# Performance work log

Measured on AMD Instinct MI355X. Metric: run time of the kernel, lower is better.

## Reference

```python
import jax, jax.numpy as jnp
import numpy as np


def _gcn_conv(x, edge_index, W, b):
    """PyG-style GCNConv: h = x @ W; out = D^-1/2 (A+I) D^-1/2 h + b."""
    N = x.shape[0]
    h = x @ W  # [N, F_out]
    # add self loops
    loops = jnp.arange(N, dtype=edge_index.dtype)
    src = jnp.concatenate([edge_index[0], loops])  # [E+N]
    dst = jnp.concatenate([edge_index[1], loops])  # [E+N]
    # symmetric normalization based on in-degree (incl. self loops)
    deg = jnp.zeros((N,), dtype=h.dtype).at[dst].add(1.0)
    dinv = jnp.where(deg > 0, jax.lax.rsqrt(deg), 0.0)
    norm = dinv[src] * dinv[dst]  # [E+N]
    # gather -> scale -> scatter-add
    msgs = h[src] * norm[:, None]  # [E+N, F_out]
    out = jax.ops.segment_sum(msgs, dst, num_segments=N)
    return out + b


def setup_inputs() -> dict:
    key = jax.random.key(0)
    k1, k2, k3, k4 = jax.random.split(key, 4)
    N, E, Cin, Ch, Cout = 50000, 800000, 128, 128, 64
    x = jax.random.normal(k1, (N, Cin), dtype=jnp.float32)
    edge_index = jax.random.randint(k2, (2, E), 0, N, dtype=jnp.int64)
    W1 = jax.random.normal(k3, (Cin, Ch), dtype=jnp.float32) / np.sqrt(Cin)
    b1 = jnp.zeros((Ch,), dtype=jnp.float32)
    W2 = jax.random.normal(k4, (Ch, Cout), dtype=jnp.float32) / np.sqrt(Ch)
    b2 = jnp.zeros((Cout,), dtype=jnp.float32)
    return {"x": x, "edge_index": edge_index, "W1": W1, "b1": b1, "W2": W2, "b2": b2}


def reference(x, edge_index, W1, b1, W2, b2):
    h = jax.nn.relu(_gcn_conv(x, edge_index, W1, b1))
    # F.dropout(training=self.training): eval mode -> identity
    return _gcn_conv(h, edge_index, W2, b2)
```

## Files before the change

### kernel.cpp

```cpp
#include <hip/hip_runtime.h>

typedef _Float16 f16;
typedef f16 f16x2 __attribute__((ext_vector_type(2)));
typedef f16 f16x8 __attribute__((ext_vector_type(8)));
typedef float f32x4 __attribute__((ext_vector_type(4)));

#define BSH 7
#define BN 128
#define CHUNK 4096
#define LCAP 4096
#define NBMAX 512
#define PMAX 512

__global__ __launch_bounds__(256) void k1(const float* __restrict__ x,
                                          const float* __restrict__ W1,
                                          const int* __restrict__ dst, f16* __restrict__ h,
                                          int* __restrict__ histG, int N, int E, int NB,
                                          int nblk) {
    __shared__ int hist[NBMAX];
    __shared__ f16 aT[64 * 136];
    __shared__ f16 bT[128 * 136];
    const int t = threadIdx.x;

    if ((int)blockIdx.x < nblk) {
        const int blk = blockIdx.x;
        for (int i = t; i < NB; i += 256) hist[i] = 0;
        __syncthreads();
        int lo = blk * CHUNK, hi = min(lo + CHUNK, E);
        for (int i = lo + t; i < hi; i += 256) atomicAdd(&hist[dst[i] >> BSH], 1);
        __syncthreads();
        for (int i = t; i < NB; i += 256) histG[(size_t)i * nblk + blk] = hist[i];
        return;
    }

    const int gb = blockIdx.x - nblk;
    const int row0 = gb * 64;
    {
        int r = t >> 2, s = (t & 3) * 32;
        bool ok = (row0 + r) < N;
        const float* xp = x + (size_t)(row0 + r) * 128 + s;
        f16* dp = &aT[r * 136 + s];
#pragma unroll
        for (int c = 0; c < 4; ++c) {
            f16x8 hv;
            if (ok) {
                float4 f0 = *(const float4*)(xp + c * 8);
                float4 f1 = *(const float4*)(xp + c * 8 + 4);
                hv[0] = (f16)f0.x; hv[1] = (f16)f0.y; hv[2] = (f16)f0.z; hv[3] = (f16)f0.w;
                hv[4] = (f16)f1.x; hv[5] = (f16)f1.y; hv[6] = (f16)f1.z; hv[7] = (f16)f1.w;
            } else {
#pragma unroll
                for (int j = 0; j < 8; ++j) hv[j] = (f16)0.f;
            }
            *(f16x8*)(dp + c * 8) = hv;
        }
    }
    for (int idx = t; idx < 128 * 128; idx += 256) {
        int k = idx >> 7, n = idx & 127;
        bT[n * 136 + k] = (f16)W1[idx];
    }
    __syncthreads();

    const int w = t >> 6, lane = t & 63, m15 = lane & 15, quad = lane >> 4;
    f32x4 acc[8];
#pragma unroll
    for (int c = 0; c < 8; ++c) acc[c] = (f32x4){0.f, 0.f, 0.f, 0.f};
    const f16* ar = &aT[(w * 16 + m15) * 136 + quad * 8];
#pragma unroll
    for (int k0 = 0; k0 < 128; k0 += 32) {
        f16x8 a = *(const f16x8*)(ar + k0);
#pragma unroll
        for (int c = 0; c < 8; ++c) {
            f16x8 b = *(const f16x8*)(&bT[(c * 16 + m15) * 136 + k0 + quad * 8]);
            acc[c] = __builtin_amdgcn_mfma_f32_16x16x32_f16(a, b, acc[c], 0, 0, 0);
        }
    }
#pragma unroll
    for (int c = 0; c < 8; ++c)
#pragma unroll
        for (int r = 0; r < 4; ++r) {
            int row = row0 + w * 16 + quad * 4 + r;
            if (row < N) h[(size_t)row * 128 + c * 16 + m15] = (f16)acc[c][r];
        }
}

__global__ __launch_bounds__(256) void scanA(int* __restrict__ a, int* __restrict__ bsum, int L) {
    __shared__ int tmp[256];
    int tid = threadIdx.x;
    int i = blockIdx.x * 256 + tid;
    int v = (i < L) ? a[i] : 0;
    tmp[tid] = v;
    __syncthreads();
    for (int o = 1; o < 256; o <<= 1) {
        int t2 = (tid >= o) ? tmp[tid - o] : 0;
        __syncthreads();
        tmp[tid] += t2;
        __syncthreads();
    }
    if (i < L) a[i] = tmp[tid] - v;
    if (tid == 255) bsum[blockIdx.x] = tmp[255];
}

__device__ __forceinline__ void scan_partials(const int* __restrict__ bsum, int nb2,
                                              int* excl , int* work ) {
    const int t = threadIdx.x & 255;
    for (int i = t; i < PMAX; i += 256) work[i] = (i < nb2) ? bsum[i] : 0;
    __syncthreads();
    for (int o = 1; o < PMAX; o <<= 1) {
        for (int i = t; i < PMAX; i += 256) excl[i] = work[i] + ((i >= o) ? work[i - o] : 0);
        __syncthreads();
        for (int i = t; i < PMAX; i += 256) work[i] = excl[i];
        __syncthreads();
    }
    for (int i = t; i < PMAX; i += 256) excl[i] = (i == 0) ? 0 : work[i - 1];
    __syncthreads();
}

__global__ __launch_bounds__(256) void place(const int* __restrict__ src,
                                             const int* __restrict__ dst,
                                             const int* __restrict__ histG,
                                             const int* __restrict__ bsum, int nb2,
                                             int* __restrict__ sorted, int E, int NB, int nblk) {
    __shared__ int excl[PMAX];
    __shared__ int work[PMAX];
    __shared__ int ofs[NBMAX];
    const int t = threadIdx.x, blk = blockIdx.x;
    scan_partials(bsum, nb2, excl, work);
    for (int i = t; i < NB; i += 256) {
        int idx = i * nblk + blk;
        ofs[i] = histG[idx] + excl[idx >> 8];
    }
    __syncthreads();
    int lo = blk * CHUNK, hi = min(lo + CHUNK, E);
    for (int i = lo + t; i < hi; i += 256) {
        int d = dst[i];
        int pos = atomicAdd(&ofs[d >> BSH], 1);
        sorted[pos] = (src[i] << BSH) | (d & (BN - 1));
    }
}

__global__ __launch_bounds__(256) void bucket_build(const int* __restrict__ histG,
                                                    const int* __restrict__ bsum, int nb2,
                                                    const int* __restrict__ sorted,
                                                    int* __restrict__ rowstart,
                                                    float* __restrict__ dinv,
                                                    int* __restrict__ csr_src, int N, int E,
                                                    int NB, int nblk) {
    __shared__ int ent[LCAP];
    __shared__ int hist[BN];
    __shared__ int lofs[BN];
    __shared__ int excl[PMAX];
    __shared__ int work[PMAX];
    const int b = blockIdx.x, t = threadIdx.x;
    scan_partials(bsum, nb2, excl, work);

    const int i0 = b * nblk;
    const int base = histG[i0] + excl[i0 >> 8];
    const int endb = (b == NB - 1) ? E : (histG[i0 + nblk] + excl[(i0 + nblk) >> 8]);
    int total = min(endb - base, LCAP);
    if (b == 0 && t == 0) rowstart[N] = E;

    for (int i = t; i < total; i += 256) ent[i] = sorted[base + i];
    if (t < BN) hist[t] = 0;
    __syncthreads();
    for (int i = t; i < total; i += 256) atomicAdd(&hist[ent[i] & (BN - 1)], 1);
    __syncthreads();
    if (t < BN) lofs[t] = hist[t];
    __syncthreads();
    for (int o = 1; o < BN; o <<= 1) {
        int v = (t < BN && t >= o) ? lofs[t - o] : 0;
        __syncthreads();
        if (t < BN) lofs[t] += v;
        __syncthreads();
    }
    if (t < BN) {
        int ex = lofs[t] - hist[t];
        int node = (b << BSH) + t;
        if (node < N) {
            rowstart[node] = base + ex;
            dinv[node] = rsqrtf((float)hist[t] + 1.0f);
        }
        lofs[t] = ex;
    }
    __syncthreads();
    for (int i = t; i < total; i += 256) {
        int e = ent[i];
        int pos = atomicAdd(&lofs[e & (BN - 1)], 1);
        csr_src[base + pos] = e >> BSH;
    }
}

__global__ __launch_bounds__(256) void gather1(const int* __restrict__ rowstart,
                                               const int* __restrict__ csr_src,
                                               const float* __restrict__ dinv,
                                               const f16* __restrict__ h,
                                               const float* __restrict__ b1,
                                               f16* __restrict__ r1, int N) {
    int node = (blockIdx.x * 256 + threadIdx.x) >> 6;
    int lane = threadIdx.x & 63;
    if (node >= N) return;
    int beg = rowstart[node], end = rowstart[node + 1];
    float dn = dinv[node];
    const f16x2* hv = (const f16x2*)h;

    f16x2 sv = hv[(size_t)node * 64 + lane];
    float ax = dn * (float)sv[0], ay = dn * (float)sv[1];
    int i = beg;
    for (; i + 4 <= end; i += 4) {
        int s0 = csr_src[i], s1 = csr_src[i + 1], s2 = csr_src[i + 2], s3 = csr_src[i + 3];
        float w0 = dinv[s0], w1 = dinv[s1], w2 = dinv[s2], w3 = dinv[s3];
        f16x2 v0 = hv[(size_t)s0 * 64 + lane];
        f16x2 v1 = hv[(size_t)s1 * 64 + lane];
        f16x2 v2 = hv[(size_t)s2 * 64 + lane];
        f16x2 v3 = hv[(size_t)s3 * 64 + lane];
        ax = fmaf(w0, (float)v0[0], ax); ay = fmaf(w0, (float)v0[1], ay);
        ax = fmaf(w1, (float)v1[0], ax); ay = fmaf(w1, (float)v1[1], ay);
        ax = fmaf(w2, (float)v2[0], ax); ay = fmaf(w2, (float)v2[1], ay);
        ax = fmaf(w3, (float)v3[0], ax); ay = fmaf(w3, (float)v3[1], ay);
    }
    for (; i < end; ++i) {
        int s = csr_src[i];
        float w = dinv[s];
        f16x2 v = hv[(size_t)s * 64 + lane];
        ax = fmaf(w, (float)v[0], ax);
        ay = fmaf(w, (float)v[1], ay);
    }
    float2 bb = ((const float2*)b1)[lane];
    float ox = fmaxf(fmaf(dn, ax, bb.x), 0.f);
    float oy = fmaxf(fmaf(dn, ay, bb.y), 0.f);
    ((f16x2*)r1)[(size_t)node * 64 + lane] = (f16x2){(f16)ox, (f16)oy};
}

__global__ __launch_bounds__(256) void gemm2(const f16* __restrict__ r1,
                                             const float* __restrict__ W2, f16* __restrict__ h2,
                                             int N) {
    __shared__ f16 aT[64 * 136];
    __shared__ f16 bT[64 * 136];
    const int t = threadIdx.x;
    const int row0 = blockIdx.x * 64;
    {
        int r = t >> 2, s = (t & 3) * 32;
        bool ok = (row0 + r) < N;
        const f16* rp = r1 + (size_t)(row0 + r) * 128 + s;
        f16* dp = &aT[r * 136 + s];
#pragma unroll
        for (int c = 0; c < 4; ++c) {
            f16x8 hv;
            if (ok) hv = *(const f16x8*)(rp + c * 8);
            else {
#pragma unroll
                for (int j = 0; j < 8; ++j) hv[j] = (f16)0.f;
            }
            *(f16x8*)(dp + c * 8) = hv;
        }
    }
    for (int idx = t; idx < 128 * 64; idx += 256) {
        int k = idx >> 6, n = idx & 63;
        bT[n * 136 + k] = (f16)W2[idx];
    }
    __syncthreads();

    const int w = t >> 6, lane = t & 63, m15 = lane & 15, quad = lane >> 4;
    f32x4 acc[4];
#pragma unroll
    for (int c = 0; c < 4; ++c) acc[c] = (f32x4){0.f, 0.f, 0.f, 0.f};
    const f16* ar = &aT[(w * 16 + m15) * 136 + quad * 8];
#pragma unroll
    for (int k0 = 0; k0 < 128; k0 += 32) {
        f16x8 a = *(const f16x8*)(ar + k0);
#pragma unroll
        for (int c = 0; c < 4; ++c) {
            f16x8 b = *(const f16x8*)(&bT[(c * 16 + m15) * 136 + k0 + quad * 8]);
            acc[c] = __builtin_amdgcn_mfma_f32_16x16x32_f16(a, b, acc[c], 0, 0, 0);
        }
    }
#pragma unroll
    for (int c = 0; c < 4; ++c)
#pragma unroll
        for (int r = 0; r < 4; ++r) {
            int row = row0 + w * 16 + quad * 4 + r;
            if (row < N) h2[(size_t)row * 64 + c * 16 + m15] = (f16)acc[c][r];
        }
}

__global__ __launch_bounds__(256) void gather2(const int* __restrict__ rowstart,
                                               const int* __restrict__ csr_src,
                                               const float* __restrict__ dinv,
                                               const f16* __restrict__ h2,
                                               const float* __restrict__ b2,
                                               float* __restrict__ out, int N) {
    int pair = (blockIdx.x * 256 + threadIdx.x) >> 6;
    int lane = threadIdx.x & 63;
    int sub = lane >> 5, l32 = lane & 31;
    int node = pair * 2 + sub;
    if (node >= N) return;
    int beg = rowstart[node], end = rowstart[node + 1];
    float dn = dinv[node];
    const f16x2* h2v = (const f16x2*)h2;

    f16x2 sv = h2v[(size_t)node * 32 + l32];
    float ax = dn * (float)sv[0], ay = dn * (float)sv[1];
    int i = beg;
    for (; i + 4 <= end; i += 4) {
        int s0 = csr_src[i], s1 = csr_src[i + 1], s2 = csr_src[i + 2], s3 = csr_src[i + 3];
        float w0 = dinv[s0], w1 = dinv[s1], w2 = dinv[s2], w3 = dinv[s3];
        f16x2 v0 = h2v[(size_t)s0 * 32 + l32];
        f16x2 v1 = h2v[(size_t)s1 * 32 + l32];
        f16x2 v2 = h2v[(size_t)s2 * 32 + l32];
        f16x2 v3 = h2v[(size_t)s3 * 32 + l32];
        ax = fmaf(w0, (float)v0[0], ax); ay = fmaf(w0, (float)v0[1], ay);
        ax = fmaf(w1, (float)v1[0], ax); ay = fmaf(w1, (float)v1[1], ay);
        ax = fmaf(w2, (float)v2[0], ax); ay = fmaf(w2, (float)v2[1], ay);
        ax = fmaf(w3, (float)v3[0], ax); ay = fmaf(w3, (float)v3[1], ay);
    }
    for (; i < end; ++i) {
        int s = csr_src[i];
        float w = dinv[s];
        f16x2 v = h2v[(size_t)s * 32 + l32];
        ax = fmaf(w, (float)v[0], ax);
        ay = fmaf(w, (float)v[1], ay);
    }
    float2 bb = ((const float2*)b2)[l32];
    float2 o;
    o.x = fmaf(dn, ax, bb.x);
    o.y = fmaf(dn, ay, bb.y);
    ((float2*)out)[(size_t)node * 32 + l32] = o;
}

extern "C" void kernel_launch(void* const* d_in, const int* in_sizes, int n_in,
                              void* d_out, int out_size, void* d_ws, size_t ws_size,
                              hipStream_t stream) {
    const float* x  = (const float*)d_in[0];
    const int*   ei = (const int*)d_in[1];
    const float* W1 = (const float*)d_in[2];
    const float* b1 = (const float*)d_in[3];
    const float* W2 = (const float*)d_in[4];
    const float* b2 = (const float*)d_in[5];

    const int N = in_sizes[0] / 128;
    const int E = in_sizes[1] / 2;
    const int* src = ei;
    const int* dst = ei + E;
    const int NB   = (N + BN - 1) >> BSH;
    const int nblk = (E + CHUNK - 1) / CHUNK;
    const int L    = NB * nblk;
    const int nb2  = (L + 255) / 256;

    char* p = (char*)d_ws;
    auto bump = [&](size_t bytes) {
        char* r = p;
        p += (bytes + 255) & ~(size_t)255;
        return r;
    };
    int*   histG    = (int*)bump((size_t)L * 4);
    int*   bsum     = (int*)bump((size_t)nb2 * 4);
    int*   sorted   = (int*)bump((size_t)E * 4);
    int*   rowstart = (int*)bump((size_t)(N + 1) * 4);
    float* dinv     = (float*)bump((size_t)N * 4);
    int*   csr_src  = (int*)bump((size_t)E * 4);
    f16*   h        = (f16*)bump((size_t)N * 128 * 2);
    f16*   r1       = (f16*)bump((size_t)N * 128 * 2);
    f16*   h2       = (f16*)bump((size_t)N * 64 * 2);
    float* out      = (float*)d_out;

    k1<<<nblk + (N + 63) / 64, 256, 0, stream>>>(x, W1, dst, h, histG, N, E, NB, nblk);
    scanA<<<nb2, 256, 0, stream>>>(histG, bsum, L);
    place<<<nblk, 256, 0, stream>>>(src, dst, histG, bsum, nb2, sorted, E, NB, nblk);
    bucket_build<<<NB, 256, 0, stream>>>(histG, bsum, nb2, sorted, rowstart, dinv, csr_src, N, E,
                                         NB, nblk);
    gather1<<<(N + 3) / 4, 256, 0, stream>>>(rowstart, csr_src, dinv, h, b1, r1, N);
    gemm2<<<(N + 63) / 64, 256, 0, stream>>>(r1, W2, h2, N);
    gather2<<<(N / 2 + 3) / 4, 256, 0, stream>>>(rowstart, csr_src, dinv, h2, b2, out, N);
}
```

Baseline: 194.0 us.

## Build CSR with global atomics and prescale features by source dinv

Measured after the change: 233.4 us. 1.2x slower.

```diff
diff --git a/kernel.cpp b/kernel.cpp
--- a/kernel.cpp
+++ b/kernel.cpp
@@ -5,34 +5,102 @@
 typedef f16 f16x8 __attribute__((ext_vector_type(8)));
 typedef float f32x4 __attribute__((ext_vector_type(4)));
 
-#define BSH 7
-#define BN 128
 #define CHUNK 4096
-#define LCAP 4096
-#define NBMAX 512
 #define PMAX 512
+
+__global__ __launch_bounds__(256) void degk(const int* __restrict__ dst, int* __restrict__ deg,
+                                            int E) {
+    int i = (blockIdx.x * 256 + threadIdx.x) * 4;
+    if (i + 4 <= E) {
+        int4 d = *(const int4*)(dst + i);
+        atomicAdd(&deg[d.x], 1);
+        atomicAdd(&deg[d.y], 1);
+        atomicAdd(&deg[d.z], 1);
+        atomicAdd(&deg[d.w], 1);
+    } else if (i < E) {
+        for (; i < E; ++i) atomicAdd(&deg[dst[i]], 1);
+    }
+}
+
+__global__ __launch_bounds__(256) void scanA(const int* __restrict__ in, int* __restrict__ outx,
+                                             int* __restrict__ bsum, int L) {
+    __shared__ int tmp[256];
+    int tid = threadIdx.x;
+    int i = blockIdx.x * 256 + tid;
+    int v = (i < L) ? in[i] : 0;
+    tmp[tid] = v;
+    __syncthreads();
+    for (int o = 1; o < 256; o <<= 1) {
+        int t2 = (tid >= o) ? tmp[tid - o] : 0;
+        __syncthreads();
+        tmp[tid] += t2;
+        __syncthreads();
+    }
+    if (i < L) outx[i] = tmp[tid] - v;
+    if (tid == 255) bsum[blockIdx.x] = tmp[255];
+}
+
+__device__ __forceinline__ void scan_partials(const int* __restrict__ bsum, int nb2,
+                                              int* excl , int* work ) {
+    const int t = threadIdx.x & 255;
+    for (int i = t; i < PMAX; i += 256) work[i] = (i < nb2) ? bsum[i] : 0;
+    __syncthreads();
+    for (int o = 1; o < PMAX; o <<= 1) {
+        for (int i = t; i < PMAX; i += 256) excl[i] = work[i] + ((i >= o) ? work[i - o] : 0);
+        __syncthreads();
+        for (int i = t; i < PMAX; i += 256) work[i] = excl[i];
+        __syncthreads();
+    }
+    for (int i = t; i < PMAX; i += 256) excl[i] = (i == 0) ? 0 : work[i - 1];
+    __syncthreads();
+}
+
+__global__ __launch_bounds__(256) void finalize(const int* __restrict__ rowscan,
+                                                const int* __restrict__ bsum, int nb2,
+                                                const int* __restrict__ deg,
+                                                int* __restrict__ rowstart, int* __restrict__ ofs,
+                                                float* __restrict__ dinv, int N, int E) {
+    __shared__ int excl[PMAX];
+    __shared__ int work[PMAX];
+    scan_partials(bsum, nb2, excl, work);
+    int i = blockIdx.x * 256 + threadIdx.x;
+    if (i < N) {
+        int rs = rowscan[i] + excl[blockIdx.x];
+        rowstart[i] = rs;
+        ofs[i] = rs;
+        dinv[i] = rsqrtf((float)deg[i] + 1.0f);
+    }
+    if (i == 0) rowstart[N] = E;
+}
 
 __global__ __launch_bounds__(256) void k1(const float* __restrict__ x,
                                           const float* __restrict__ W1,
-                                          const int* __restrict__ dst, f16* __restrict__ h,
-                                          int* __restrict__ histG, int N, int E, int NB,
-                                          int nblk) {
-    __shared__ int hist[NBMAX];
+                                          const int* __restrict__ src, const int* __restrict__ dst,
+                                          int* __restrict__ ofs, int* __restrict__ csr_src,
+                                          const float* __restrict__ dinv, f16* __restrict__ h,
+                                          int N, int E, int nblk) {
+    const int t = threadIdx.x;
+
+    if ((int)blockIdx.x < nblk) {
+        const int base = blockIdx.x * CHUNK;
+        const int n = min(CHUNK, E - base);
+        for (int j = t * 4; j + 4 <= n; j += 1024) {
+            int4 d4 = *(const int4*)(dst + base + j);
+            int4 s4 = *(const int4*)(src + base + j);
+            csr_src[atomicAdd(&ofs[d4.x], 1)] = s4.x;
+            csr_src[atomicAdd(&ofs[d4.y], 1)] = s4.y;
+            csr_src[atomicAdd(&ofs[d4.z], 1)] = s4.z;
+            csr_src[atomicAdd(&ofs[d4.w], 1)] = s4.w;
+        }
+        if (t == 0) {
+            for (int j = n & ~3; j < n; ++j)
+                csr_src[atomicAdd(&ofs[dst[base + j]], 1)] = src[base + j];
+        }
+        return;
+    }
+
     __shared__ f16 aT[64 * 136];
     __shared__ f16 bT[128 * 136];
-    const int t = threadIdx.x;
-
-    if ((int)blockIdx.x < nblk) {
-        const int blk = blockIdx.x;
-        for (int i = t; i < NB; i += 256) hist[i] = 0;
-        __syncthreads();
-        int lo = blk * CHUNK, hi = min(lo + CHUNK, E);
-        for (int i = lo + t; i < hi; i += 256) atomicAdd(&hist[dst[i] >> BSH], 1);
-        __syncthreads();
-        for (int i = t; i < NB; i += 256) histG[(size_t)i * nblk + blk] = hist[i];
-        return;
-    }
-
     const int gb = blockIdx.x - nblk;
     const int row0 = gb * 64;
     {
@@ -75,119 +143,20 @@
             acc[c] = __builtin_amdgcn_mfma_f32_16x16x32_f16(a, b, acc[c], 0, 0, 0);
         }
     }
+    const int rbase = row0 + w * 16 + quad * 4;
+    float dv[4];
+#pragma unroll
+    for (int r = 0; r < 4; ++r) {
+        int row = rbase + r;
+        dv[r] = (row < N) ? dinv[row] : 0.f;
+    }
 #pragma unroll
     for (int c = 0; c < 8; ++c)
 #pragma unroll
         for (int r = 0; r < 4; ++r) {
-            int row = row0 + w * 16 + quad * 4 + r;
-            if (row < N) h[(size_t)row * 128 + c * 16 + m15] = (f16)acc[c][r];
-        }
-}
-
-__global__ __launch_bounds__(256) void scanA(int* __restrict__ a, int* __restrict__ bsum, int L) {
-    __shared__ int tmp[256];
-    int tid = threadIdx.x;
-    int i = blockIdx.x * 256 + tid;
-    int v = (i < L) ? a[i] : 0;
-    tmp[tid] = v;
-    __syncthreads();
-    for (int o = 1; o < 256; o <<= 1) {
-        int t2 = (tid >= o) ? tmp[tid - o] : 0;
-        __syncthreads();
-        tmp[tid] += t2;
-        __syncthreads();
-    }
-    if (i < L) a[i] = tmp[tid] - v;
-    if (tid == 255) bsum[blockIdx.x] = tmp[255];
-}
-
-__device__ __forceinline__ void scan_partials(const int* __restrict__ bsum, int nb2,
-                                              int* excl , int* work ) {
-    const int t = threadIdx.x & 255;
-    for (int i = t; i < PMAX; i += 256) work[i] = (i < nb2) ? bsum[i] : 0;
-    __syncthreads();
-    for (int o = 1; o < PMAX; o <<= 1) {
-        for (int i = t; i < PMAX; i += 256) excl[i] = work[i] + ((i >= o) ? work[i - o] : 0);
-        __syncthreads();
-        for (int i = t; i < PMAX; i += 256) work[i] = excl[i];
-        __syncthreads();
-    }
-    for (int i = t; i < PMAX; i += 256) excl[i] = (i == 0) ? 0 : work[i - 1];
-    __syncthreads();
-}
-
-__global__ __launch_bounds__(256) void place(const int* __restrict__ src,
-                                             const int* __restrict__ dst,
-                                             const int* __restrict__ histG,
-                                             const int* __restrict__ bsum, int nb2,
-                                             int* __restrict__ sorted, int E, int NB, int nblk) {
-    __shared__ int excl[PMAX];
-    __shared__ int work[PMAX];
-    __shared__ int ofs[NBMAX];
-    const int t = threadIdx.x, blk = blockIdx.x;
-    scan_partials(bsum, nb2, excl, work);
-    for (int i = t; i < NB; i += 256) {
-        int idx = i * nblk + blk;
-        ofs[i] = histG[idx] + excl[idx >> 8];
-    }
-    __syncthreads();
-    int lo = blk * CHUNK, hi = min(lo + CHUNK, E);
-    for (int i = lo + t; i < hi; i += 256) {
-        int d = dst[i];
-        int pos = atomicAdd(&ofs[d >> BSH], 1);
-        sorted[pos] = (src[i] << BSH) | (d & (BN - 1));
-    }
-}
-
-__global__ __launch_bounds__(256) void bucket_build(const int* __restrict__ histG,
-                                                    const int* __restrict__ bsum, int nb2,
-                                                    const int* __restrict__ sorted,
-                                                    int* __restrict__ rowstart,
-                                                    float* __restrict__ dinv,
-                                                    int* __restrict__ csr_src, int N, int E,
-                                                    int NB, int nblk) {
-    __shared__ int ent[LCAP];
-    __shared__ int hist[BN];
-    __shared__ int lofs[BN];
-    __shared__ int excl[PMAX];
-    __shared__ int work[PMAX];
-    const int b = blockIdx.x, t = threadIdx.x;
-    scan_partials(bsum, nb2, excl, work);
-
-    const int i0 = b * nblk;
-    const int base = histG[i0] + excl[i0 >> 8];
-    const int endb = (b == NB - 1) ? E : (histG[i0 + nblk] + excl[(i0 + nblk) >> 8]);
-    int total = min(endb - base, LCAP);
-    if (b == 0 && t == 0) rowstart[N] = E;
-
-    for (int i = t; i < total; i += 256) ent[i] = sorted[base + i];
-    if (t < BN) hist[t] = 0;
-    __syncthreads();
-    for (int i = t; i < total; i += 256) atomicAdd(&hist[ent[i] & (BN - 1)], 1);
-    __syncthreads();
-    if (t < BN) lofs[t] = hist[t];
-    __syncthreads();
-    for (int o = 1; o < BN; o <<= 1) {
-        int v = (t < BN && t >= o) ? lofs[t - o] : 0;
-        __syncthreads();
-        if (t < BN) lofs[t] += v;
-        __syncthreads();
-    }
-    if (t < BN) {
-        int ex = lofs[t] - hist[t];
-        int node = (b << BSH) + t;
-        if (node < N) {
-            rowstart[node] = base + ex;
-            dinv[node] = rsqrtf((float)hist[t] + 1.0f);
-        }
-        lofs[t] = ex;
-    }
-    __syncthreads();
-    for (int i = t; i < total; i += 256) {
-        int e = ent[i];
-        int pos = atomicAdd(&lofs[e & (BN - 1)], 1);
-        csr_src[base + pos] = e >> BSH;
-    }
+            int row = rbase + r;
+            if (row < N) h[(size_t)row * 128 + c * 16 + m15] = (f16)(acc[c][r] * dv[r]);
+        }
 }
 
 __global__ __launch_bounds__(256) void gather1(const int* __restrict__ rowstart,
@@ -196,7 +165,7 @@
                                                const f16* __restrict__ h,
                                                const float* __restrict__ b1,
                                                f16* __restrict__ r1, int N) {
-    int node = (blockIdx.x * 256 + threadIdx.x) >> 6;
+    int node = __builtin_amdgcn_readfirstlane((int)((blockIdx.x * 256 + threadIdx.x) >> 6));
     int lane = threadIdx.x & 63;
     if (node >= N) return;
     int beg = rowstart[node], end = rowstart[node + 1];
@@ -204,30 +173,28 @@
     const f16x2* hv = (const f16x2*)h;
 
     f16x2 sv = hv[(size_t)node * 64 + lane];
-    float ax = dn * (float)sv[0], ay = dn * (float)sv[1];
+    float ax = (float)sv[0], ay = (float)sv[1];
     int i = beg;
     for (; i + 4 <= end; i += 4) {
         int s0 = csr_src[i], s1 = csr_src[i + 1], s2 = csr_src[i + 2], s3 = csr_src[i + 3];
-        float w0 = dinv[s0], w1 = dinv[s1], w2 = dinv[s2], w3 = dinv[s3];
         f16x2 v0 = hv[(size_t)s0 * 64 + lane];
         f16x2 v1 = hv[(size_t)s1 * 64 + lane];
         f16x2 v2 = hv[(size_t)s2 * 64 + lane];
         f16x2 v3 = hv[(size_t)s3 * 64 + lane];
-        ax = fmaf(w0, (float)v0[0], ax); ay = fmaf(w0, (float)v0[1], ay);
-        ax = fmaf(w1, (float)v1[0], ax); ay = fmaf(w1, (float)v1[1], ay);
-        ax = fmaf(w2, (float)v2[0], ax); ay = fmaf(w2, (float)v2[1], ay);
-        ax = fmaf(w3, (float)v3[0], ax); ay = fmaf(w3, (float)v3[1], ay);
+        ax += (float)v0[0]; ay += (float)v0[1];
+        ax += (float)v1[0]; ay += (float)v1[1];
+        ax += (float)v2[0]; ay += (float)v2[1];
+        ax += (float)v3[0]; ay += (float)v3[1];
     }
     for (; i < end; ++i) {
         int s = csr_src[i];
-        float w = dinv[s];
         f16x2 v = hv[(size_t)s * 64 + lane];
-        ax = fmaf(w, (float)v[0], ax);
-        ay = fmaf(w, (float)v[1], ay);
+        ax += (float)v[0];
+        ay += (float)v[1];
     }
     float2 bb = ((const float2*)b1)[lane];
-    float ox = fmaxf(fmaf(dn, ax, bb.x), 0.f);
-    float oy = fmaxf(fmaf(dn, ay, bb.y), 0.f);
+    float ox = dn * fmaxf(fmaf(dn, ax, bb.x), 0.f);
+    float oy = dn * fmaxf(fmaf(dn, ay, bb.y), 0.f);
     ((f16x2*)r1)[(size_t)node * 64 + lane] = (f16x2){(f16)ox, (f16)oy};
 }
 
@@ -299,26 +266,24 @@
     const f16x2* h2v = (const f16x2*)h2;
 
     f16x2 sv = h2v[(size_t)node * 32 + l32];
-    float ax = dn * (float)sv[0], ay = dn * (float)sv[1];
+    float ax = (float)sv[0], ay = (float)sv[1];
     int i = beg;
     for (; i + 4 <= end; i += 4) {
         int s0 = csr_src[i], s1 = csr_src[i + 1], s2 = csr_src[i + 2], s3 = csr_src[i + 3];
-        float w0 = dinv[s0], w1 = dinv[s1], w2 = dinv[s2], w3 = dinv[s3];
         f16x2 v0 = h2v[(size_t)s0 * 32 + l32];
         f16x2 v1 = h2v[(size_t)s1 * 32 + l32];
         f16x2 v2 = h2v[(size_t)s2 * 32 + l32];
         f16x2 v3 = h2v[(size_t)s3 * 32 + l32];
-        ax = fmaf(w0, (float)v0[0], ax); ay = fmaf(w0, (float)v0[1], ay);
-        ax = fmaf(w1, (float)v1[0], ax); ay = fmaf(w1, (float)v1[1], ay);
-        ax = fmaf(w2, (float)v2[0], ax); ay = fmaf(w2, (float)v2[1], ay);
-        ax = fmaf(w3, (float)v3[0], ax); ay = fmaf(w3, (float)v3[1], ay);
+        ax += (float)v0[0]; ay += (float)v0[1];
+        ax += (float)v1[0]; ay += (float)v1[1];
+        ax += (float)v2[0]; ay += (float)v2[1];
+        ax += (float)v3[0]; ay += (float)v3[1];
     }
     for (; i < end; ++i) {
         int s = csr_src[i];
-        float w = dinv[s];
         f16x2 v = h2v[(size_t)s * 32 + l32];
-        ax = fmaf(w, (float)v[0], ax);
-        ay = fmaf(w, (float)v[1], ay);
+        ax += (float)v[0];
+        ay += (float)v[1];
     }
     float2 bb = ((const float2*)b2)[l32];
     float2 o;
@@ -341,10 +306,8 @@
     const int E = in_sizes[1] / 2;
     const int* src = ei;
     const int* dst = ei + E;
-    const int NB   = (N + BN - 1) >> BSH;
     const int nblk = (E + CHUNK - 1) / CHUNK;
-    const int L    = NB * nblk;
-    const int nb2  = (L + 255) / 256;
+    const int nb2  = (N + 255) / 256;
 
     char* p = (char*)d_ws;
     auto bump = [&](size_t bytes) {
@@ -352,10 +315,11 @@
         p += (bytes + 255) & ~(size_t)255;
         return r;
     };
-    int*   histG    = (int*)bump((size_t)L * 4);
+    int*   deg      = (int*)bump((size_t)N * 4);
+    int*   rowscan  = (int*)bump((size_t)N * 4);
     int*   bsum     = (int*)bump((size_t)nb2 * 4);
-    int*   sorted   = (int*)bump((size_t)E * 4);
     int*   rowstart = (int*)bump((size_t)(N + 1) * 4);
+    int*   ofs      = (int*)bump((size_t)N * 4);
     float* dinv     = (float*)bump((size_t)N * 4);
     int*   csr_src  = (int*)bump((size_t)E * 4);
     f16*   h        = (f16*)bump((size_t)N * 128 * 2);
@@ -363,11 +327,12 @@
     f16*   h2       = (f16*)bump((size_t)N * 64 * 2);
     float* out      = (float*)d_out;
 
-    k1<<<nblk + (N + 63) / 64, 256, 0, stream>>>(x, W1, dst, h, histG, N, E, NB, nblk);
-    scanA<<<nb2, 256, 0, stream>>>(histG, bsum, L);
-    place<<<nblk, 256, 0, stream>>>(src, dst, histG, bsum, nb2, sorted, E, NB, nblk);
-    bucket_build<<<NB, 256, 0, stream>>>(histG, bsum, nb2, sorted, rowstart, dinv, csr_src, N, E,
-                                         NB, nblk);
+    hipMemsetAsync(deg, 0, (size_t)N * 4, stream);
+    degk<<<(E / 4 + 255) / 256, 256, 0, stream>>>(dst, deg, E);
+    scanA<<<nb2, 256, 0, stream>>>(deg, rowscan, bsum, N);
+    finalize<<<nb2, 256, 0, stream>>>(rowscan, bsum, nb2, deg, rowstart, ofs, dinv, N, E);
+    k1<<<nblk + (N + 63) / 64, 256, 0, stream>>>(x, W1, src, dst, ofs, csr_src, dinv, h, N, E,
+                                                 nblk);
     gather1<<<(N + 3) / 4, 256, 0, stream>>>(rowstart, csr_src, dinv, h, b1, r1, N);
     gemm2<<<(N + 63) / 64, 256, 0, stream>>>(r1, W2, h2, N);
     gather2<<<(N / 2 + 3) / 4, 256, 0, stream>>>(rowstart, csr_src, dinv, h2, b2, out, N);
```

## Restructure pipeline: fuse place with GEMM1, pre-transpose weights, fold dinv into gather1

Applied to the files above, without the earlier changes.

Result: faster. 181.3 us, median of 2 (-6.6%).

```diff
diff --git a/kernel.cpp b/kernel.cpp
--- a/kernel.cpp
+++ b/kernel.cpp
@@ -2,6 +2,7 @@
 
 typedef _Float16 f16;
 typedef f16 f16x2 __attribute__((ext_vector_type(2)));
+typedef f16 f16x4 __attribute__((ext_vector_type(4)));
 typedef f16 f16x8 __attribute__((ext_vector_type(8)));
 typedef float f32x4 __attribute__((ext_vector_type(4)));
 
@@ -12,24 +13,100 @@
 #define NBMAX 512
 #define PMAX 512
 
+__global__ __launch_bounds__(256) void degh(const int* __restrict__ dst, int* __restrict__ histG,
+                                            const float* __restrict__ W1,
+                                            const float* __restrict__ W2, f16* __restrict__ w1t,
+                                            f16* __restrict__ w2t, int E, int NB, int nblk) {
+    const int t = threadIdx.x, blk = blockIdx.x;
+    if (blk < nblk) {
+        __shared__ int hist[NBMAX];
+        for (int i = t; i < NB; i += 256) hist[i] = 0;
+        __syncthreads();
+        int lo = blk * CHUNK, hi = min(lo + CHUNK, E);
+        for (int i = lo + t; i < hi; i += 256) atomicAdd(&hist[dst[i] >> BSH], 1);
+        __syncthreads();
+        for (int i = t; i < NB; i += 256) histG[(size_t)i * nblk + blk] = hist[i];
+        return;
+    }
+    if (blk == nblk) {
+        for (int idx = t; idx < 128 * 128; idx += 256) {
+            int n = idx >> 7, k = idx & 127;
+            w1t[idx] = (f16)W1[k * 128 + n];
+        }
+        return;
+    }
+    for (int idx = t; idx < 64 * 128; idx += 256) {
+        int n = idx >> 7, k = idx & 127;
+        w2t[idx] = (f16)W2[k * 64 + n];
+    }
+}
+
+__global__ __launch_bounds__(256) void scanA(int* __restrict__ a, int* __restrict__ bsum, int L) {
+    __shared__ int tmp[256];
+    int tid = threadIdx.x;
+    int i = blockIdx.x * 256 + tid;
+    int v = (i < L) ? a[i] : 0;
+    tmp[tid] = v;
+    __syncthreads();
+    for (int o = 1; o < 256; o <<= 1) {
+        int t2 = (tid >= o) ? tmp[tid - o] : 0;
+        __syncthreads();
+        tmp[tid] += t2;
+        __syncthreads();
+    }
+    if (i < L) a[i] = tmp[tid] - v;
+    if (tid == 255) bsum[blockIdx.x] = tmp[255];
+}
+
+__device__ __forceinline__ void scan_partials(const int* __restrict__ bsum, int nb2,
+                                              int* excl , int* work ) {
+    const int t = threadIdx.x & 255;
+    for (int i = t; i < PMAX; i += 256) work[i] = (i < nb2) ? bsum[i] : 0;
+    __syncthreads();
+    for (int o = 1; o < PMAX; o <<= 1) {
+        for (int i = t; i < PMAX; i += 256) excl[i] = work[i] + ((i >= o) ? work[i - o] : 0);
+        __syncthreads();
+        for (int i = t; i < PMAX; i += 256) work[i] = excl[i];
+        __syncthreads();
+    }
+    for (int i = t; i < PMAX; i += 256) excl[i] = (i == 0) ? 0 : work[i - 1];
+    __syncthreads();
+}
+
 __global__ __launch_bounds__(256) void k1(const float* __restrict__ x,
-                                          const float* __restrict__ W1,
-                                          const int* __restrict__ dst, f16* __restrict__ h,
-                                          int* __restrict__ histG, int N, int E, int NB,
-                                          int nblk) {
-    __shared__ int hist[NBMAX];
-    __shared__ f16 aT[64 * 136];
-    __shared__ f16 bT[128 * 136];
+                                          const f16* __restrict__ w1t,
+                                          const int* __restrict__ src, const int* __restrict__ dst,
+                                          const int* __restrict__ histG,
+                                          const int* __restrict__ bsum, int nb2,
+                                          int* __restrict__ sorted, f16* __restrict__ h, int N,
+                                          int E, int NB, int nblk) {
+    __shared__ union SM {
+        struct {
+            f16 aT[64 * 136];
+            f16 bT[128 * 136];
+        } g;
+        struct {
+            int excl[PMAX];
+            int work[PMAX];
+            int ofs[NBMAX];
+        } p;
+    } sm;
     const int t = threadIdx.x;
 
     if ((int)blockIdx.x < nblk) {
         const int blk = blockIdx.x;
-        for (int i = t; i < NB; i += 256) hist[i] = 0;
+        scan_partials(bsum, nb2, sm.p.excl, sm.p.work);
+        for (int i = t; i < NB; i += 256) {
+            int idx = i * nblk + blk;
+            sm.p.ofs[i] = histG[idx] + sm.p.excl[idx >> 8];
+        }
         __syncthreads();
         int lo = blk * CHUNK, hi = min(lo + CHUNK, E);
-        for (int i = lo + t; i < hi; i += 256) atomicAdd(&hist[dst[i] >> BSH], 1);
-        __syncthreads();
-        for (int i = t; i < NB; i += 256) histG[(size_t)i * nblk + blk] = hist[i];
+        for (int i = lo + t; i < hi; i += 256) {
+            int d = dst[i];
+            int pos = atomicAdd(&sm.p.ofs[d >> BSH], 1);
+            sorted[pos] = (src[i] << BSH) | (d & (BN - 1));
+        }
         return;
     }
 
@@ -39,7 +116,7 @@
         int r = t >> 2, s = (t & 3) * 32;
         bool ok = (row0 + r) < N;
         const float* xp = x + (size_t)(row0 + r) * 128 + s;
-        f16* dp = &aT[r * 136 + s];
+        f16* dp = &sm.g.aT[r * 136 + s];
 #pragma unroll
         for (int c = 0; c < 4; ++c) {
             f16x8 hv;
@@ -55,9 +132,9 @@
             *(f16x8*)(dp + c * 8) = hv;
         }
     }
-    for (int idx = t; idx < 128 * 128; idx += 256) {
-        int k = idx >> 7, n = idx & 127;
-        bT[n * 136 + k] = (f16)W1[idx];
+    for (int idx = t; idx < 128 * 16; idx += 256) {
+        int n = idx >> 4, c = idx & 15;
+        *(f16x8*)&sm.g.bT[n * 136 + c * 8] = *(const f16x8*)&w1t[n * 128 + c * 8];
     }
     __syncthreads();
 
@@ -65,13 +142,13 @@
     f32x4 acc[8];
 #pragma unroll
     for (int c = 0; c < 8; ++c) acc[c] = (f32x4){0.f, 0.f, 0.f, 0.f};
-    const f16* ar = &aT[(w * 16 + m15) * 136 + quad * 8];
+    const f16* ar = &sm.g.aT[(w * 16 + m15) * 136 + quad * 8];
 #pragma unroll
     for (int k0 = 0; k0 < 128; k0 += 32) {
         f16x8 a = *(const f16x8*)(ar + k0);
 #pragma unroll
         for (int c = 0; c < 8; ++c) {
-            f16x8 b = *(const f16x8*)(&bT[(c * 16 + m15) * 136 + k0 + quad * 8]);
+            f16x8 b = *(const f16x8*)(&sm.g.bT[(c * 16 + m15) * 136 + k0 + quad * 8]);
             acc[c] = __builtin_amdgcn_mfma_f32_16x16x32_f16(a, b, acc[c], 0, 0, 0);
         }
     }
@@ -82,61 +159,6 @@
             int row = row0 + w * 16 + quad * 4 + r;
             if (row < N) h[(size_t)row * 128 + c * 16 + m15] = (f16)acc[c][r];
         }
-}
-
-__global__ __launch_bounds__(256) void scanA(int* __restrict__ a, int* __restrict__ bsum, int L) {
-    __shared__ int tmp[256];
-    int tid = threadIdx.x;
-    int i = blockIdx.x * 256 + tid;
-    int v = (i < L) ? a[i] : 0;
-    tmp[tid] = v;
-    __syncthreads();
-    for (int o = 1; o < 256; o <<= 1) {
-        int t2 = (tid >= o) ? tmp[tid - o] : 0;
-        __syncthreads();
-        tmp[tid] += t2;
-        __syncthreads();
-    }
-    if (i < L) a[i] = tmp[tid] - v;
-    if (tid == 255) bsum[blockIdx.x] = tmp[255];
-}
-
-__device__ __forceinline__ void scan_partials(const int* __restrict__ bsum, int nb2,
-                                              int* excl , int* work ) {
-    const int t = threadIdx.x & 255;
-    for (int i = t; i < PMAX; i += 256) work[i] = (i < nb2) ? bsum[i] : 0;
-    __syncthreads();
-    for (int o = 1; o < PMAX; o <<= 1) {
-        for (int i = t; i < PMAX; i += 256) excl[i] = work[i] + ((i >= o) ? work[i - o] : 0);
-        __syncthreads();
-        for (int i = t; i < PMAX; i += 256) work[i] = excl[i];
-        __syncthreads();
-    }
-    for (int i = t; i < PMAX; i += 256) excl[i] = (i == 0) ? 0 : work[i - 1];
-    __syncthreads();
-}
-
-__global__ __launch_bounds__(256) void place(const int* __restrict__ src,
-                                             const int* __restrict__ dst,
-                                             const int* __restrict__ histG,
-                                             const int* __restrict__ bsum, int nb2,
-                                             int* __restrict__ sorted, int E, int NB, int nblk) {
-    __shared__ int excl[PMAX];
-    __shared__ int work[PMAX];
-    __shared__ int ofs[NBMAX];
-    const int t = threadIdx.x, blk = blockIdx.x;
-    scan_partials(bsum, nb2, excl, work);
-    for (int i = t; i < NB; i += 256) {
-        int idx = i * nblk + blk;
-        ofs[i] = histG[idx] + excl[idx >> 8];
-    }
-    __syncthreads();
-    int lo = blk * CHUNK, hi = min(lo + CHUNK, E);
-    for (int i = lo + t; i < hi; i += 256) {
-        int d = dst[i];
-        int pos = atomicAdd(&ofs[d >> BSH], 1);
-        sorted[pos] = (src[i] << BSH) | (d & (BN - 1));
-    }
 }
 
 __global__ __launch_bounds__(256) void bucket_build(const int* __restrict__ histG,
@@ -196,43 +218,52 @@
                                                const f16* __restrict__ h,
                                                const float* __restrict__ b1,
                                                f16* __restrict__ r1, int N) {
-    int node = (blockIdx.x * 256 + threadIdx.x) >> 6;
+    int wid = (blockIdx.x * 256 + threadIdx.x) >> 6;
     int lane = threadIdx.x & 63;
+    int sub = lane >> 5, l32 = lane & 31;
+    int node = wid * 2 + sub;
     if (node >= N) return;
     int beg = rowstart[node], end = rowstart[node + 1];
     float dn = dinv[node];
-    const f16x2* hv = (const f16x2*)h;
-
-    f16x2 sv = hv[(size_t)node * 64 + lane];
-    float ax = dn * (float)sv[0], ay = dn * (float)sv[1];
+    const f16x4* hv = (const f16x4*)h;
+
+    f16x4 sv = hv[(size_t)node * 32 + l32];
+    float a0 = dn * (float)sv[0], a1 = dn * (float)sv[1];
+    float a2 = dn * (float)sv[2], a3 = dn * (float)sv[3];
     int i = beg;
     for (; i + 4 <= end; i += 4) {
         int s0 = csr_src[i], s1 = csr_src[i + 1], s2 = csr_src[i + 2], s3 = csr_src[i + 3];
         float w0 = dinv[s0], w1 = dinv[s1], w2 = dinv[s2], w3 = dinv[s3];
-        f16x2 v0 = hv[(size_t)s0 * 64 + lane];
-        f16x2 v1 = hv[(size_t)s1 * 64 + lane];
-        f16x2 v2 = hv[(size_t)s2 * 64 + lane];
-        f16x2 v3 = hv[(size_t)s3 * 64 + lane];
-        ax = fmaf(w0, (float)v0[0], ax); ay = fmaf(w0, (float)v0[1], ay);
-        ax = fmaf(w1, (float)v1[0], ax); ay = fmaf(w1, (float)v1[1], ay);
-        ax = fmaf(w2, (float)v2[0], ax); ay = fmaf(w2, (float)v2[1], ay);
-        ax = fmaf(w3, (float)v3[0], ax); ay = fmaf(w3, (float)v3[1], ay);
+        f16x4 v0 = hv[(size_t)s0 * 32 + l32];
+        f16x4 v1 = hv[(size_t)s1 * 32 + l32];
+        f16x4 v2 = hv[(size_t)s2 * 32 + l32];
+        f16x4 v3 = hv[(size_t)s3 * 32 + l32];
+        a0 = fmaf(w0, (float)v0[0], a0); a1 = fmaf(w0, (float)v0[1], a1);
+        a2 = fmaf(w0, (float)v0[2], a2); a3 = fmaf(w0, (float)v0[3], a3);
+        a0 = fmaf(w1, (float)v1[0], a0); a1 = fmaf(w1, (float)v1[1], a1);
+        a2 = fmaf(w1, (float)v1[2], a2); a3 = fmaf(w1, (float)v1[3], a3);
+        a0 = fmaf(w2, (float)v2[0], a0); a1 = fmaf(w2, (float)v2[1], a1);
+        a2 = fmaf(w2, (float)v2[2], a2); a3 = fmaf(w2, (float)v2[3], a3);
+        a0 = fmaf(w3, (float)v3[0], a0); a1 = fmaf(w3, (float)v3[1], a1);
+        a2 = fmaf(w3, (float)v3[2], a2); a3 = fmaf(w3, (float)v3[3], a3);
     }
     for (; i < end; ++i) {
         int s = csr_src[i];
         float w = dinv[s];
-        f16x2 v = hv[(size_t)s * 64 + lane];
-        ax = fmaf(w, (float)v[0], ax);
-        ay = fmaf(w, (float)v[1], ay);
-    }
-    float2 bb = ((const float2*)b1)[lane];
-    float ox = fmaxf(fmaf(dn, ax, bb.x), 0.f);
-    float oy = fmaxf(fmaf(dn, ay, bb.y), 0.f);
-    ((f16x2*)r1)[(size_t)node * 64 + lane] = (f16x2){(f16)ox, (f16)oy};
+        f16x4 v = hv[(size_t)s * 32 + l32];
+        a0 = fmaf(w, (float)v[0], a0); a1 = fmaf(w, (float)v[1], a1);
+        a2 = fmaf(w, (float)v[2], a2); a3 = fmaf(w, (float)v[3], a3);
+    }
+    float4 bb = ((const float4*)b1)[l32];
+    float o0 = dn * fmaxf(fmaf(dn, a0, bb.x), 0.f);
+    float o1 = dn * fmaxf(fmaf(dn, a1, bb.y), 0.f);
+    float o2 = dn * fmaxf(fmaf(dn, a2, bb.z), 0.f);
+    float o3 = dn * fmaxf(fmaf(dn, a3, bb.w), 0.f);
+    ((f16x4*)r1)[(size_t)node * 32 + l32] = (f16x4){(f16)o0, (f16)o1, (f16)o2, (f16)o3};
 }
 
 __global__ __launch_bounds__(256) void gemm2(const f16* __restrict__ r1,
-                                             const float* __restrict__ W2, f16* __restrict__ h2,
+                                             const f16* __restrict__ w2t, f16* __restrict__ h2,
                                              int N) {
     __shared__ f16 aT[64 * 136];
     __shared__ f16 bT[64 * 136];
@@ -254,9 +285,9 @@
             *(f16x8*)(dp + c * 8) = hv;
         }
     }
-    for (int idx = t; idx < 128 * 64; idx += 256) {
-        int k = idx >> 6, n = idx & 63;
-        bT[n * 136 + k] = (f16)W2[idx];
+    for (int idx = t; idx < 64 * 16; idx += 256) {
+        int n = idx >> 4, c = idx & 15;
+        *(f16x8*)&bT[n * 136 + c * 8] = *(const f16x8*)&w2t[n * 128 + c * 8];
     }
     __syncthreads();
 
@@ -289,42 +320,41 @@
                                                const f16* __restrict__ h2,
                                                const float* __restrict__ b2,
                                                float* __restrict__ out, int N) {
-    int pair = (blockIdx.x * 256 + threadIdx.x) >> 6;
+    int wid = (blockIdx.x * 256 + threadIdx.x) >> 6;
     int lane = threadIdx.x & 63;
-    int sub = lane >> 5, l32 = lane & 31;
-    int node = pair * 2 + sub;
+    int q = lane >> 4, l16 = lane & 15;
+    int node = wid * 4 + q;
     if (node >= N) return;
     int beg = rowstart[node], end = rowstart[node + 1];
     float dn = dinv[node];
-    const f16x2* h2v = (const f16x2*)h2;
-
-    f16x2 sv = h2v[(size_t)node * 32 + l32];
-    float ax = dn * (float)sv[0], ay = dn * (float)sv[1];
+    const f16x4* h2v = (const f16x4*)h2;
+
+    f16x4 sv = h2v[(size_t)node * 16 + l16];
+    float a0 = (float)sv[0], a1 = (float)sv[1], a2 = (float)sv[2], a3 = (float)sv[3];
     int i = beg;
     for (; i + 4 <= end; i += 4) {
         int s0 = csr_src[i], s1 = csr_src[i + 1], s2 = csr_src[i + 2], s3 = csr_src[i + 3];
-        float w0 = dinv[s0], w1 = dinv[s1], w2 = dinv[s2], w3 = dinv[s3];
-        f16x2 v0 = h2v[(size_t)s0 * 32 + l32];
-        f16x2 v1 = h2v[(size_t)s1 * 32 + l32];
-        f16x2 v2 = h2v[(size_t)s2 * 32 + l32];
-        f16x2 v3 = h2v[(size_t)s3 * 32 + l32];
-        ax = fmaf(w0, (float)v0[0], ax); ay = fmaf(w0, (float)v0[1], ay);
-        ax = fmaf(w1, (float)v1[0], ax); ay = fmaf(w1, (float)v1[1], ay);
-        ax = fmaf(w2, (float)v2[0], ax); ay = fmaf(w2, (float)v2[1], ay);
-        ax = fmaf(w3, (float)v3[0], ax); ay = fmaf(w3, (float)v3[1], ay);
+        f16x4 v0 = h2v[(size_t)s0 * 16 + l16];
+        f16x4 v1 = h2v[(size_t)s1 * 16 + l16];
+        f16x4 v2 = h2v[(size_t)s2 * 16 + l16];
+        f16x4 v3 = h2v[(size_t)s3 * 16 + l16];
+        a0 += (float)v0[0]; a1 += (float)v0[1]; a2 += (float)v0[2]; a3 += (float)v0[3];
+        a0 += (float)v1[0]; a1 += (float)v1[1]; a2 += (float)v1[2]; a3 += (float)v1[3];
+        a0 += (float)v2[0]; a1 += (float)v2[1]; a2 += (float)v2[2]; a3 += (float)v2[3];
+        a0 += (float)v3[0]; a1 += (float)v3[1]; a2 += (float)v3[2]; a3 += (float)v3[3];
     }
     for (; i < end; ++i) {
         int s = csr_src[i];
-        float w = dinv[s];
-        f16x2 v = h2v[(size_t)s * 32 + l32];
-        ax = fmaf(w, (float)v[0], ax);
-        ay = fmaf(w, (float)v[1], ay);
-    }
-    float2 bb = ((const float2*)b2)[l32];
-    float2 o;
-    o.x = fmaf(dn, ax, bb.x);
-    o.y = fmaf(dn, ay, bb.y);
-    ((float2*)out)[(size_t)node * 32 + l32] = o;
+        f16x4 v = h2v[(size_t)s * 16 + l16];
+        a0 += (float)v[0]; a1 += (float)v[1]; a2 += (float)v[2]; a3 += (float)v[3];
+    }
+    float4 bb = ((const float4*)b2)[l16];
+    float4 o;
+    o.x = fmaf(dn, a0, bb.x);
+    o.y = fmaf(dn, a1, bb.y);
+    o.z = fmaf(dn, a2, bb.z);
+    o.w = fmaf(dn, a3, bb.w);
+    ((float4*)out)[(size_t)node * 16 + l16] = o;
 }
 
 extern "C" void kernel_launch(void* const* d_in, const int* in_sizes, int n_in,
@@ -361,14 +391,17 @@
     f16*   h        = (f16*)bump((size_t)N * 128 * 2);
     f16*   r1       = (f16*)bump((size_t)N * 128 * 2);
     f16*   h2       = (f16*)bump((size_t)N * 64 * 2);
+    f16*   w1t      = (f16*)bump((size_t)128 * 128 * 2);
+    f16*   w2t      = (f16*)bump((size_t)64 * 128 * 2);
     float* out      = (float*)d_out;
 
-    k1<<<nblk + (N + 63) / 64, 256, 0, stream>>>(x, W1, dst, h, histG, N, E, NB, nblk);
+    degh<<<nblk + 2, 256, 0, stream>>>(dst, histG, W1, W2, w1t, w2t, E, NB, nblk);
     scanA<<<nb2, 256, 0, stream>>>(histG, bsum, L);
-    place<<<nblk, 256, 0, stream>>>(src, dst, histG, bsum, nb2, sorted, E, NB, nblk);
+    k1<<<nblk + (N + 63) / 64, 256, 0, stream>>>(x, w1t, src, dst, histG, bsum, nb2, sorted, h, N,
+                                                 E, NB, nblk);
     bucket_build<<<NB, 256, 0, stream>>>(histG, bsum, nb2, sorted, rowstart, dinv, csr_src, N, E,
                                          NB, nblk);
-    gather1<<<(N + 3) / 4, 256, 0, stream>>>(rowstart, csr_src, dinv, h, b1, r1, N);
-    gemm2<<<(N + 63) / 64, 256, 0, stream>>>(r1, W2, h2, N);
-    gather2<<<(N / 2 + 3) / 4, 256, 0, stream>>>(rowstart, csr_src, dinv, h2, b2, out, N);
-}
+    gather1<<<((N + 1) / 2 + 3) / 4, 256, 0, stream>>>(rowstart, csr_src, dinv, h, b1, r1, N);
+    gemm2<<<(N + 63) / 64, 256, 0, stream>>>(r1, w2t, h2, N);
+    gather2<<<((N + 3) / 4 + 3) / 4, 256, 0, stream>>>(rowstart, csr_src, dinv, h2, b2, out, N);
+}
```
